# Optimization experiments

Hardware: AMD Instinct MI355X
Metric: run time of the kernel (lower is better)

## Reference

```python
import jax, jax.numpy as jnp
import numpy as np

LATENT = 768
HEADS = 12
HEAD_DIM = LATENT // HEADS
FFN = 4 * LATENT


def setup_inputs() -> dict:
    key = jax.random.key(0)
    ks = jax.random.split(key, 16)
    s = 1.0 / np.sqrt(LATENT)
    inp = {
        "x": jax.random.normal(ks[0], (2, 2048, LATENT), dtype=jnp.float32),
        "Wq": jax.random.normal(ks[1], (LATENT, LATENT), dtype=jnp.float32) * s,
        "bq": jnp.zeros((LATENT,), jnp.float32),
        "Wk": jax.random.normal(ks[2], (LATENT, LATENT), dtype=jnp.float32) * s,
        "bk": jnp.zeros((LATENT,), jnp.float32),
        "Wv": jax.random.normal(ks[3], (LATENT, LATENT), dtype=jnp.float32) * s,
        "bv": jnp.zeros((LATENT,), jnp.float32),
        "Wo": jax.random.normal(ks[4], (LATENT, LATENT), dtype=jnp.float32) * s,
        "bo": jnp.zeros((LATENT,), jnp.float32),
        "ln1_g": jnp.ones((LATENT,), jnp.float32),
        "ln1_b": jnp.zeros((LATENT,), jnp.float32),
        "ln2_g": jnp.ones((LATENT,), jnp.float32),
        "ln2_b": jnp.zeros((LATENT,), jnp.float32),
        "W1": jax.random.normal(ks[5], (FFN, LATENT), dtype=jnp.float32) * s,
        "b1": jnp.zeros((FFN,), jnp.float32),
        "W2": jax.random.normal(ks[6], (LATENT, FFN), dtype=jnp.float32) * (1.0 / np.sqrt(FFN)),
        "b2": jnp.zeros((LATENT,), jnp.float32),
    }
    return inp


def _layernorm(x, g, b, eps=1e-5):
    mu = jnp.mean(x, axis=-1, keepdims=True)
    var = jnp.var(x, axis=-1, keepdims=True)
    return (x - mu) * jax.lax.rsqrt(var + eps) * g + b


def reference(x, Wq, bq, Wk, bk, Wv, bv, Wo, bo, ln1_g, ln1_b, ln2_g, ln2_b, W1, b1, W2, b2):
    b, n, d = x.shape
    # torch Linear: y = x @ W.T + bias
    Q = (x @ Wq.T + bq).reshape(b, n, HEADS, HEAD_DIM).transpose(0, 2, 1, 3)
    K = (x @ Wk.T + bk).reshape(b, n, HEADS, HEAD_DIM).transpose(0, 2, 1, 3)
    V = (x @ Wv.T + bv).reshape(b, n, HEADS, HEAD_DIM).transpose(0, 2, 1, 3)
    scores = jnp.einsum("bhqd,bhkd->bhqk", Q, K) / np.sqrt(HEAD_DIM)  # [b,h,n,n]
    weights = jax.nn.softmax(scores, axis=-1)
    attn = jnp.einsum("bhqk,bhkd->bhqd", weights, V)
    attn = attn.transpose(0, 2, 1, 3).reshape(b, n, d)
    attn = attn @ Wo.T + bo
    x = _layernorm(x + attn, ln1_g, ln1_b)
    h = jax.nn.gelu(x @ W1.T + b1, approximate=False)
    ffn = h @ W2.T + b2
    x = _layernorm(x + ffn, ln2_g, ln2_b)
    return x
```

## Files before the change

kernel.cpp:

```cpp
#include <hip/hip_runtime.h>
#include <hip/hip_bf16.h>
#include <cstddef>
#include <cstdint>

typedef __bf16 bf16_t;
typedef bf16_t bf16x8 __attribute__((ext_vector_type(8)));
typedef bf16_t bf16x4 __attribute__((ext_vector_type(4)));
typedef float f32x4 __attribute__((ext_vector_type(4)));

#define LATENT 768
#define FFN_DIM 3072
#define NTOK 4096
#define SEQ 2048
#define HEADS 12
#define HD 64

__device__ __forceinline__ void gload_lds16(const bf16_t* g, bf16_t* l) {
    __builtin_amdgcn_global_load_lds((const __attribute__((address_space(1))) void*)g,
                                     (__attribute__((address_space(3))) void*)l, 16, 0, 0);
}

struct CvtDesc {
    const float* src[7];
    bf16_t* dst[7];
    int n4[7];
};

__global__ __launch_bounds__(256) void cvt_f32_bf16(CvtDesc d) {
    int seg = blockIdx.y;
    int i = blockIdx.x * 256 + threadIdx.x;
    if (i >= d.n4[seg]) return;
    float4 v = ((const float4*)d.src[seg])[i];
    bf16x4 o;
    o[0] = (bf16_t)v.x; o[1] = (bf16_t)v.y; o[2] = (bf16_t)v.z; o[3] = (bf16_t)v.w;
    *(bf16x4*)&d.dst[seg][(size_t)i * 4] = o;
}

template<int EPI, int NT>
__global__ __launch_bounds__(256) void gemm128(const bf16_t* __restrict__ A,
                                               const bf16_t* __restrict__ B,
                                               const float* __restrict__ bias,
                                               void* __restrict__ Cv,
                                               int M, int N, int K) {
    __shared__ __align__(16) bf16_t As[128 * 32];
    __shared__ __align__(16) bf16_t Bs[NT * 32];
    const int NJ = NT / 32;
    int t = threadIdx.x;
    int w = t >> 6;
    int lane = t & 63, l16 = lane & 15, quad = lane >> 4;
    int m0 = blockIdx.x * 128, n0 = blockIdx.y * NT;
    int mrow0 = (w & 1) * 64, ncol0 = (w >> 1) * (NT / 2);

    f32x4 acc[4][NJ] = {};

    int srow = lane >> 2;
    int sseg = (lane & 3) * 8;

    for (int k0 = 0; k0 < K; k0 += 32) {
        __syncthreads();
        const bf16_t* Ag = A + (size_t)(m0 + w * 32 + srow) * K + k0 + sseg;
        gload_lds16(Ag,          &As[(w * 32) * 32]);
        gload_lds16(Ag + 16 * K, &As[(w * 32 + 16) * 32]);
        if (NT == 128) {
            const bf16_t* Bg = B + (size_t)(n0 + w * 32 + srow) * K + k0 + sseg;
            gload_lds16(Bg,          &Bs[(w * 32) * 32]);
            gload_lds16(Bg + 16 * K, &Bs[(w * 32 + 16) * 32]);
        } else {
            const bf16_t* Bg = B + (size_t)(n0 + w * 16 + srow) * K + k0 + sseg;
            gload_lds16(Bg, &Bs[(w * 16) * 32]);
        }
        __syncthreads();

        bf16x8 a[4], b[NJ];
#pragma unroll
        for (int i = 0; i < 4; ++i)
            a[i] = *(const bf16x8*)&As[(mrow0 + i * 16 + l16) * 32 + quad * 8];
#pragma unroll
        for (int j = 0; j < NJ; ++j)
            b[j] = *(const bf16x8*)&Bs[(ncol0 + j * 16 + l16) * 32 + quad * 8];
#pragma unroll
        for (int i = 0; i < 4; ++i)
#pragma unroll
            for (int j = 0; j < NJ; ++j)
                acc[i][j] = __builtin_amdgcn_mfma_f32_16x16x32_bf16(a[i], b[j], acc[i][j], 0, 0, 0);
    }

    float* Cf = (float*)Cv;
    bf16_t* Cb = (bf16_t*)Cv;
#pragma unroll
    for (int j = 0; j < NJ; ++j) {
        int col = n0 + ncol0 + j * 16 + l16;
        float bvv = bias[col];
#pragma unroll
        for (int i = 0; i < 4; ++i) {
            int row0 = m0 + mrow0 + i * 16 + quad * 4;
#pragma unroll
            for (int r = 0; r < 4; ++r) {
                float v = acc[i][j][r] + bvv;
                if (EPI == 2) v = 0.5f * v * (1.0f + erff(v * 0.70710678118654752f));
                if (EPI == 0) Cf[(size_t)(row0 + r) * N + col] = v;
                else          Cb[(size_t)(row0 + r) * N + col] = (bf16_t)v;
            }
        }
    }
}

__global__ __launch_bounds__(256) void v_transpose(const bf16_t* __restrict__ QKV,
                                                   bf16_t* __restrict__ Vt) {
    __shared__ bf16_t Ts[64][68];
    int t = threadIdx.x;
    int bh = blockIdx.y;
    int b = bh / HEADS, h = bh % HEADS;
    int n0 = blockIdx.x * 64;
    size_t rowbase = (size_t)b * SEQ;
    int r = t >> 3, seg = (t & 7) * 8;
#pragma unroll
    for (int i = 0; i < 2; ++i) {
        int rr = r + i * 32;
        *(bf16x8*)&Ts[rr][seg] =
            *(const bf16x8*)&QKV[(rowbase + n0 + rr) * (3 * LATENT) + 2 * LATENT + h * HD + seg];
    }
    __syncthreads();
#pragma unroll
    for (int i = 0; i < 2; ++i) {
        int d = r + i * 32;
        bf16x8 o;
#pragma unroll
        for (int jj = 0; jj < 8; ++jj) o[jj] = Ts[seg + jj][d];
        *(bf16x8*)&Vt[((size_t)bh * HD + d) * SEQ + n0 + seg] = o;
    }
}

__global__ __launch_bounds__(256) void attn_flash(const bf16_t* __restrict__ QKV,
                                                  const bf16_t* __restrict__ Vt,
                                                  bf16_t* __restrict__ O) {
    __shared__ __align__(16) bf16_t Ks[2][64][32];
    __shared__ __align__(16) bf16_t Vts[2][64][32];
    __shared__ __align__(16) bf16_t Ps[4][32][72];

    int t = threadIdx.x;
    int w = t >> 6;
    int lane = t & 63, l16 = lane & 15, quad = lane >> 4;
    int bh = blockIdx.y;
    int b = bh / HEADS, h = bh % HEADS;
    size_t rowbase = (size_t)b * SEQ;
    int qw = blockIdx.x * 128 + w * 32;
    const int LD = 3 * LATENT;
    const float C2 = 0.125f * 1.44269504088896f;

    bf16x8 aq[2][2];
#pragma unroll
    for (int mi = 0; mi < 2; ++mi) {
        const bf16_t* qrow = QKV + (rowbase + qw + mi * 16 + l16) * LD + h * HD;
        aq[mi][0] = *(const bf16x8*)&qrow[quad * 8];
        aq[mi][1] = *(const bf16x8*)&qrow[32 + quad * 8];
    }

    f32x4 accd[2][4] = {};
    f32x4 vsum[2] = {};

    int c = w & 1, half = w >> 1;
    int srow = lane >> 2, sseg = (lane & 3) * 8;

    for (int kt = 0; kt < SEQ / 64; ++kt) {
        __syncthreads();
        {
            int krow = half * 32 + srow;
            const bf16_t* kg = QKV + (rowbase + kt * 64 + krow) * LD + LATENT + h * HD + c * 32 + sseg;
            gload_lds16(kg,           &Ks[c][half * 32][0]);
            gload_lds16(kg + 16 * LD, &Ks[c][half * 32 + 16][0]);
            const bf16_t* vg = Vt + ((size_t)bh * HD + half * 32 + srow) * SEQ + kt * 64 + c * 32 + sseg;
            gload_lds16(vg,            &Vts[c][half * 32][0]);
            gload_lds16(vg + 16 * SEQ, &Vts[c][half * 32 + 16][0]);
        }
        __syncthreads();

        bf16x8 bk[4][2];
#pragma unroll
        for (int si = 0; si < 4; ++si)
#pragma unroll
            for (int cc = 0; cc < 2; ++cc)
                bk[si][cc] = *(const bf16x8*)&Ks[cc][si * 16 + l16][quad * 8];

#pragma unroll
        for (int mi = 0; mi < 2; ++mi) {
#pragma unroll
            for (int si = 0; si < 4; ++si) {
                f32x4 z = {};
#pragma unroll
                for (int cc = 0; cc < 2; ++cc)
                    z = __builtin_amdgcn_mfma_f32_16x16x32_bf16(aq[mi][cc], bk[si][cc], z, 0, 0, 0);
#pragma unroll
                for (int r = 0; r < 4; ++r) {
                    float p = __builtin_amdgcn_exp2f(z[r] * C2);
                    vsum[mi][r] += p;
                    Ps[w][mi * 16 + quad * 4 + r][si * 16 + l16] = (bf16_t)p;
                }
            }
        }
        __threadfence_block();

        bf16x8 ap[2][2];
#pragma unroll
        for (int mi = 0; mi < 2; ++mi)
#pragma unroll
            for (int cc = 0; cc < 2; ++cc)
                ap[mi][cc] = *(const bf16x8*)&Ps[w][mi * 16 + l16][cc * 32 + quad * 8];

        bf16x8 bv[4][2];
#pragma unroll
        for (int dt = 0; dt < 4; ++dt)
#pragma unroll
            for (int cc = 0; cc < 2; ++cc)
                bv[dt][cc] = *(const bf16x8*)&Vts[cc][dt * 16 + l16][quad * 8];

#pragma unroll
        for (int mi = 0; mi < 2; ++mi)
#pragma unroll
            for (int dt = 0; dt < 4; ++dt)
#pragma unroll
                for (int cc = 0; cc < 2; ++cc)
                    accd[mi][dt] = __builtin_amdgcn_mfma_f32_16x16x32_bf16(ap[mi][cc], bv[dt][cc], accd[mi][dt], 0, 0, 0);
    }

#pragma unroll
    for (int mi = 0; mi < 2; ++mi) {
#pragma unroll
        for (int off = 1; off < 16; off <<= 1)
#pragma unroll
            for (int r = 0; r < 4; ++r) vsum[mi][r] += __shfl_xor(vsum[mi][r], off, 64);
    }
    f32x4 rinv[2];
#pragma unroll
    for (int mi = 0; mi < 2; ++mi)
#pragma unroll
        for (int r = 0; r < 4; ++r) rinv[mi][r] = 1.0f / vsum[mi][r];

#pragma unroll
    for (int mi = 0; mi < 2; ++mi)
#pragma unroll
        for (int dt = 0; dt < 4; ++dt)
#pragma unroll
            for (int r = 0; r < 4; ++r) {
                size_t row = rowbase + qw + mi * 16 + quad * 4 + r;
                O[row * LATENT + h * HD + dt * 16 + l16] = (bf16_t)(accd[mi][dt][r] * rinv[mi][r]);
            }
}

__global__ __launch_bounds__(256) void ln_residual(const float* __restrict__ base,
                                                   const float* __restrict__ add,
                                                   const float* __restrict__ g,
                                                   const float* __restrict__ bta,
                                                   float* __restrict__ outf,
                                                   bf16_t* __restrict__ outb) {
    int row = blockIdx.x;
    const float* xr = base + (size_t)row * LATENT;
    const float* ar = add + (size_t)row * LATENT;
    int t = threadIdx.x;
    float v[3];
    float s = 0.f;
#pragma unroll
    for (int i = 0; i < 3; ++i) {
        v[i] = xr[t + i * 256] + ar[t + i * 256];
        s += v[i];
    }
    __shared__ float red[4];
#pragma unroll
    for (int off = 1; off < 64; off <<= 1) s += __shfl_xor(s, off, 64);
    if ((t & 63) == 0) red[t >> 6] = s;
    __syncthreads();
    float mu = (red[0] + red[1] + red[2] + red[3]) * (1.f / LATENT);
    float q = 0.f;
#pragma unroll
    for (int i = 0; i < 3; ++i) {
        float d = v[i] - mu;
        q += d * d;
    }
#pragma unroll
    for (int off = 1; off < 64; off <<= 1) q += __shfl_xor(q, off, 64);
    __syncthreads();
    if ((t & 63) == 0) red[t >> 6] = q;
    __syncthreads();
    float var = (red[0] + red[1] + red[2] + red[3]) * (1.f / LATENT);
    float rs = rsqrtf(var + 1e-5f);
#pragma unroll
    for (int i = 0; i < 3; ++i) {
        int cix = t + i * 256;
        float o = (v[i] - mu) * rs * g[cix] + bta[cix];
        outf[(size_t)row * LATENT + cix] = o;
        if (outb) outb[(size_t)row * LATENT + cix] = (bf16_t)o;
    }
}

extern "C" void kernel_launch(void* const* d_in, const int* in_sizes, int n_in,
                              void* d_out, int out_size, void* d_ws, size_t ws_size,
                              hipStream_t stream) {
    const float* x   = (const float*)d_in[0];
    const float* Wq  = (const float*)d_in[1];
    const float* bq  = (const float*)d_in[2];
    const float* Wk  = (const float*)d_in[3];
    const float* bk  = (const float*)d_in[4];
    const float* Wv  = (const float*)d_in[5];
    const float* bv  = (const float*)d_in[6];
    const float* Wo  = (const float*)d_in[7];
    const float* bo  = (const float*)d_in[8];
    const float* g1  = (const float*)d_in[9];
    const float* be1 = (const float*)d_in[10];
    const float* g2  = (const float*)d_in[11];
    const float* be2 = (const float*)d_in[12];
    const float* W1  = (const float*)d_in[13];
    const float* b1  = (const float*)d_in[14];
    const float* W2  = (const float*)d_in[15];
    const float* b2  = (const float*)d_in[16];
    float* out = (float*)d_out;

    char* ws = (char*)d_ws;
    size_t off = 0;
    auto alloc = [&](size_t bytes) {
        char* p = ws + off;
        off = (off + bytes + 255) & ~(size_t)255;
        return p;
    };
    bf16_t* xbf   = (bf16_t*)alloc((size_t)NTOK * LATENT * 2);
    bf16_t* Wcat  = (bf16_t*)alloc((size_t)3 * LATENT * LATENT * 2);
    bf16_t* Wobf  = (bf16_t*)alloc((size_t)LATENT * LATENT * 2);
    bf16_t* W1bf  = (bf16_t*)alloc((size_t)FFN_DIM * LATENT * 2);
    bf16_t* W2bf  = (bf16_t*)alloc((size_t)LATENT * FFN_DIM * 2);
    float*  bcat  = (float*)alloc((size_t)3 * LATENT * 4);
    bf16_t* QKV   = (bf16_t*)alloc((size_t)NTOK * 3 * LATENT * 2);
    bf16_t* attnO = (bf16_t*)alloc((size_t)NTOK * LATENT * 2);
    float*  tmpf  = (float*)alloc((size_t)NTOK * LATENT * 4);
    float*  y1f   = (float*)alloc((size_t)NTOK * LATENT * 4);
    bf16_t* y1bf  = (bf16_t*)alloc((size_t)NTOK * LATENT * 2);
    bf16_t* hbf   = (bf16_t*)alloc((size_t)NTOK * FFN_DIM * 2);
    bf16_t* Vtg   = (bf16_t*)hbf;

    CvtDesc cd;
    cd.src[0] = x;   cd.dst[0] = xbf;                        cd.n4[0] = NTOK * LATENT / 4;
    cd.src[1] = Wq;  cd.dst[1] = Wcat;                       cd.n4[1] = LATENT * LATENT / 4;
    cd.src[2] = Wk;  cd.dst[2] = Wcat + LATENT * LATENT;     cd.n4[2] = LATENT * LATENT / 4;
    cd.src[3] = Wv;  cd.dst[3] = Wcat + 2 * LATENT * LATENT; cd.n4[3] = LATENT * LATENT / 4;
    cd.src[4] = Wo;  cd.dst[4] = Wobf;                       cd.n4[4] = LATENT * LATENT / 4;
    cd.src[5] = W1;  cd.dst[5] = W1bf;                       cd.n4[5] = FFN_DIM * LATENT / 4;
    cd.src[6] = W2;  cd.dst[6] = W2bf;                       cd.n4[6] = FFN_DIM * LATENT / 4;
    {
        int maxn4 = NTOK * LATENT / 4;
        dim3 grid((maxn4 + 255) / 256, 7);
        cvt_f32_bf16<<<grid, 256, 0, stream>>>(cd);
    }
    hipMemcpyAsync(bcat, bq, LATENT * 4, hipMemcpyDeviceToDevice, stream);
    hipMemcpyAsync(bcat + LATENT, bk, LATENT * 4, hipMemcpyDeviceToDevice, stream);
    hipMemcpyAsync(bcat + 2 * LATENT, bv, LATENT * 4, hipMemcpyDeviceToDevice, stream);

    gemm128<1, 128><<<dim3(NTOK / 128, 3 * LATENT / 128), 256, 0, stream>>>(
        xbf, Wcat, bcat, QKV, NTOK, 3 * LATENT, LATENT);

    v_transpose<<<dim3(SEQ / 64, 2 * HEADS), 256, 0, stream>>>(QKV, Vtg);

    attn_flash<<<dim3(SEQ / 128, 2 * HEADS), 256, 0, stream>>>(QKV, Vtg, attnO);

    gemm128<0, 64><<<dim3(NTOK / 128, LATENT / 64), 256, 0, stream>>>(
        attnO, Wobf, bo, tmpf, NTOK, LATENT, LATENT);

    ln_residual<<<NTOK, 256, 0, stream>>>(x, tmpf, g1, be1, y1f, y1bf);

    gemm128<2, 128><<<dim3(NTOK / 128, FFN_DIM / 128), 256, 0, stream>>>(
        y1bf, W1bf, b1, hbf, NTOK, FFN_DIM, LATENT);

    gemm128<0, 64><<<dim3(NTOK / 128, LATENT / 64), 256, 0, stream>>>(
        hbf, W2bf, b2, tmpf, NTOK, LATENT, FFN_DIM);

    ln_residual<<<NTOK, 256, 0, stream>>>(y1f, tmpf, g2, be2, out, nullptr);
}
```

Before: 338.2 us.

## Split attention KV range and output GEMMs along K into partial sums

```diff
diff --git a/kernel.cpp b/kernel.cpp
--- a/kernel.cpp
+++ b/kernel.cpp
@@ -41,7 +41,7 @@
                                                const bf16_t* __restrict__ B,
                                                const float* __restrict__ bias,
                                                void* __restrict__ Cv,
-                                               int M, int N, int K) {
+                                               int M, int N, int Klen, int Kstride) {
     __shared__ __align__(16) bf16_t As[128 * 32];
     __shared__ __align__(16) bf16_t Bs[NT * 32];
     const int NJ = NT / 32;
@@ -56,17 +56,17 @@
     int srow = lane >> 2;
     int sseg = (lane & 3) * 8;
 
-    for (int k0 = 0; k0 < K; k0 += 32) {
+    for (int k0 = 0; k0 < Klen; k0 += 32) {
         __syncthreads();
-        const bf16_t* Ag = A + (size_t)(m0 + w * 32 + srow) * K + k0 + sseg;
-        gload_lds16(Ag,          &As[(w * 32) * 32]);
-        gload_lds16(Ag + 16 * K, &As[(w * 32 + 16) * 32]);
+        const bf16_t* Ag = A + (size_t)(m0 + w * 32 + srow) * Kstride + k0 + sseg;
+        gload_lds16(Ag,                &As[(w * 32) * 32]);
+        gload_lds16(Ag + 16 * Kstride, &As[(w * 32 + 16) * 32]);
         if (NT == 128) {
-            const bf16_t* Bg = B + (size_t)(n0 + w * 32 + srow) * K + k0 + sseg;
-            gload_lds16(Bg,          &Bs[(w * 32) * 32]);
-            gload_lds16(Bg + 16 * K, &Bs[(w * 32 + 16) * 32]);
+            const bf16_t* Bg = B + (size_t)(n0 + w * 32 + srow) * Kstride + k0 + sseg;
+            gload_lds16(Bg,                &Bs[(w * 32) * 32]);
+            gload_lds16(Bg + 16 * Kstride, &Bs[(w * 32 + 16) * 32]);
         } else {
-            const bf16_t* Bg = B + (size_t)(n0 + w * 16 + srow) * K + k0 + sseg;
+            const bf16_t* Bg = B + (size_t)(n0 + w * 16 + srow) * Kstride + k0 + sseg;
             gload_lds16(Bg, &Bs[(w * 16) * 32]);
         }
         __syncthreads();
@@ -90,7 +90,7 @@
 #pragma unroll
     for (int j = 0; j < NJ; ++j) {
         int col = n0 + ncol0 + j * 16 + l16;
-        float bvv = bias[col];
+        float bvv = bias ? bias[col] : 0.0f;
 #pragma unroll
         for (int i = 0; i < 4; ++i) {
             int row0 = m0 + mrow0 + i * 16 + quad * 4;
@@ -133,7 +133,10 @@
 
 __global__ __launch_bounds__(256) void attn_flash(const bf16_t* __restrict__ QKV,
                                                   const bf16_t* __restrict__ Vt,
-                                                  bf16_t* __restrict__ O) {
+                                                  float* __restrict__ Op0,
+                                                  float* __restrict__ Op1,
+                                                  float* __restrict__ vs0,
+                                                  float* __restrict__ vs1) {
     __shared__ __align__(16) bf16_t Ks[2][64][32];
     __shared__ __align__(16) bf16_t Vts[2][64][32];
     __shared__ __align__(16) bf16_t Ps[4][32][72];
@@ -143,6 +146,9 @@
     int lane = t & 63, l16 = lane & 15, quad = lane >> 4;
     int bh = blockIdx.y;
     int b = bh / HEADS, h = bh % HEADS;
+    int z = blockIdx.z;
+    float* Op = z ? Op1 : Op0;
+    float* vs = z ? vs1 : vs0;
     size_t rowbase = (size_t)b * SEQ;
     int qw = blockIdx.x * 128 + w * 32;
     const int LD = 3 * LATENT;
@@ -162,7 +168,7 @@
     int c = w & 1, half = w >> 1;
     int srow = lane >> 2, sseg = (lane & 3) * 8;
 
-    for (int kt = 0; kt < SEQ / 64; ++kt) {
+    for (int kt = z * (SEQ / 128); kt < (z + 1) * (SEQ / 128); ++kt) {
         __syncthreads();
         {
             int krow = half * 32 + srow;
@@ -186,13 +192,13 @@
         for (int mi = 0; mi < 2; ++mi) {
 #pragma unroll
             for (int si = 0; si < 4; ++si) {
-                f32x4 z = {};
+                f32x4 z2 = {};
 #pragma unroll
                 for (int cc = 0; cc < 2; ++cc)
-                    z = __builtin_amdgcn_mfma_f32_16x16x32_bf16(aq[mi][cc], bk[si][cc], z, 0, 0, 0);
+                    z2 = __builtin_amdgcn_mfma_f32_16x16x32_bf16(aq[mi][cc], bk[si][cc], z2, 0, 0, 0);
 #pragma unroll
                 for (int r = 0; r < 4; ++r) {
-                    float p = __builtin_amdgcn_exp2f(z[r] * C2);
+                    float p = __builtin_amdgcn_exp2f(z2[r] * C2);
                     vsum[mi][r] += p;
                     Ps[w][mi * 16 + quad * 4 + r][si * 16 + l16] = (bf16_t)p;
                 }
@@ -229,12 +235,14 @@
         for (int off = 1; off < 16; off <<= 1)
 #pragma unroll
             for (int r = 0; r < 4; ++r) vsum[mi][r] += __shfl_xor(vsum[mi][r], off, 64);
-    }
-    f32x4 rinv[2];
-#pragma unroll
-    for (int mi = 0; mi < 2; ++mi)
-#pragma unroll
-        for (int r = 0; r < 4; ++r) rinv[mi][r] = 1.0f / vsum[mi][r];
+        if (l16 == 0) {
+#pragma unroll
+            for (int r = 0; r < 4; ++r) {
+                size_t tok = rowbase + qw + mi * 16 + quad * 4 + r;
+                vs[tok * HEADS + h] = vsum[mi][r];
+            }
+        }
+    }
 
 #pragma unroll
     for (int mi = 0; mi < 2; ++mi)
@@ -243,25 +251,46 @@
 #pragma unroll
             for (int r = 0; r < 4; ++r) {
                 size_t row = rowbase + qw + mi * 16 + quad * 4 + r;
-                O[row * LATENT + h * HD + dt * 16 + l16] = (bf16_t)(accd[mi][dt][r] * rinv[mi][r]);
+                Op[row * LATENT + h * HD + dt * 16 + l16] = accd[mi][dt][r];
             }
 }
 
-__global__ __launch_bounds__(256) void ln_residual(const float* __restrict__ base,
-                                                   const float* __restrict__ add,
-                                                   const float* __restrict__ g,
-                                                   const float* __restrict__ bta,
-                                                   float* __restrict__ outf,
-                                                   bf16_t* __restrict__ outb) {
+__global__ __launch_bounds__(256) void attn_combine(const float* __restrict__ Op0,
+                                                    const float* __restrict__ Op1,
+                                                    const float* __restrict__ vs0,
+                                                    const float* __restrict__ vs1,
+                                                    bf16_t* __restrict__ O) {
+    int row = blockIdx.x;
+    int t = threadIdx.x;
+    const float* a = Op0 + (size_t)row * LATENT;
+    const float* bb = Op1 + (size_t)row * LATENT;
+#pragma unroll
+    for (int i = 0; i < 3; ++i) {
+        int c = t + i * 256;
+        int h = c >> 6;
+        float denom = vs0[(size_t)row * HEADS + h] + vs1[(size_t)row * HEADS + h];
+        O[(size_t)row * LATENT + c] = (bf16_t)((a[c] + bb[c]) / denom);
+    }
+}
+
+__global__ __launch_bounds__(256) void ln_residual2(const float* __restrict__ base,
+                                                    const float* __restrict__ add1,
+                                                    const float* __restrict__ add2,
+                                                    const float* __restrict__ g,
+                                                    const float* __restrict__ bta,
+                                                    float* __restrict__ outf,
+                                                    bf16_t* __restrict__ outb) {
     int row = blockIdx.x;
     const float* xr = base + (size_t)row * LATENT;
-    const float* ar = add + (size_t)row * LATENT;
+    const float* a1 = add1 + (size_t)row * LATENT;
+    const float* a2 = add2 + (size_t)row * LATENT;
     int t = threadIdx.x;
     float v[3];
     float s = 0.f;
 #pragma unroll
     for (int i = 0; i < 3; ++i) {
-        v[i] = xr[t + i * 256] + ar[t + i * 256];
+        int c = t + i * 256;
+        v[i] = xr[c] + a1[c] + a2[c];
         s += v[i];
     }
     __shared__ float red[4];
@@ -333,7 +362,12 @@
     float*  y1f   = (float*)alloc((size_t)NTOK * LATENT * 4);
     bf16_t* y1bf  = (bf16_t*)alloc((size_t)NTOK * LATENT * 2);
     bf16_t* hbf   = (bf16_t*)alloc((size_t)NTOK * FFN_DIM * 2);
+    float*  vsa   = (float*)alloc((size_t)NTOK * HEADS * 4);
+    float*  vsb   = (float*)alloc((size_t)NTOK * HEADS * 4);
     bf16_t* Vtg   = (bf16_t*)hbf;
+    float*  Oa    = tmpf;
+    float*  Ob    = y1f;
+    float*  part2 = (float*)QKV;
 
     CvtDesc cd;
     cd.src[0] = x;   cd.dst[0] = xbf;                        cd.n4[0] = NTOK * LATENT / 4;
@@ -353,22 +387,28 @@
     hipMemcpyAsync(bcat + 2 * LATENT, bv, LATENT * 4, hipMemcpyDeviceToDevice, stream);
 
     gemm128<1, 128><<<dim3(NTOK / 128, 3 * LATENT / 128), 256, 0, stream>>>(
-        xbf, Wcat, bcat, QKV, NTOK, 3 * LATENT, LATENT);
+        xbf, Wcat, bcat, QKV, NTOK, 3 * LATENT, LATENT, LATENT);
 
     v_transpose<<<dim3(SEQ / 64, 2 * HEADS), 256, 0, stream>>>(QKV, Vtg);
 
-    attn_flash<<<dim3(SEQ / 128, 2 * HEADS), 256, 0, stream>>>(QKV, Vtg, attnO);
+    attn_flash<<<dim3(SEQ / 128, 2 * HEADS, 2), 256, 0, stream>>>(QKV, Vtg, Oa, Ob, vsa, vsb);
+
+    attn_combine<<<NTOK, 256, 0, stream>>>(Oa, Ob, vsa, vsb, attnO);
 
     gemm128<0, 64><<<dim3(NTOK / 128, LATENT / 64), 256, 0, stream>>>(
-        attnO, Wobf, bo, tmpf, NTOK, LATENT, LATENT);
-
-    ln_residual<<<NTOK, 256, 0, stream>>>(x, tmpf, g1, be1, y1f, y1bf);
+        attnO, Wobf, bo, tmpf, NTOK, LATENT, LATENT / 2, LATENT);
+    gemm128<0, 64><<<dim3(NTOK / 128, LATENT / 64), 256, 0, stream>>>(
+        attnO + LATENT / 2, Wobf + LATENT / 2, nullptr, part2, NTOK, LATENT, LATENT / 2, LATENT);
+
+    ln_residual2<<<NTOK, 256, 0, stream>>>(x, tmpf, part2, g1, be1, y1f, y1bf);
 
     gemm128<2, 128><<<dim3(NTOK / 128, FFN_DIM / 128), 256, 0, stream>>>(
-        y1bf, W1bf, b1, hbf, NTOK, FFN_DIM, LATENT);
+        y1bf, W1bf, b1, hbf, NTOK, FFN_DIM, LATENT, LATENT);
 
     gemm128<0, 64><<<dim3(NTOK / 128, LATENT / 64), 256, 0, stream>>>(
-        hbf, W2bf, b2, tmpf, NTOK, LATENT, FFN_DIM);
-
-    ln_residual<<<NTOK, 256, 0, stream>>>(y1f, tmpf, g2, be2, out, nullptr);
-}
+        hbf, W2bf, b2, tmpf, NTOK, LATENT, FFN_DIM / 2, FFN_DIM);
+    gemm128<0, 64><<<dim3(NTOK / 128, LATENT / 64), 256, 0, stream>>>(
+        hbf + FFN_DIM / 2, W2bf + FFN_DIM / 2, nullptr, part2, NTOK, LATENT, FFN_DIM / 2, FFN_DIM);
+
+    ln_residual2<<<NTOK, 256, 0, stream>>>(y1f, tmpf, part2, g2, be2, out, nullptr);
+}
```

Result: slower. 358.9 us (+6.1%).

## Split attention KV range across two blocks with single-wave blocks and combine pass

Applied to the files above, without the earlier changes.

```diff
diff --git a/kernel.cpp b/kernel.cpp
--- a/kernel.cpp
+++ b/kernel.cpp
@@ -131,20 +131,23 @@
     }
 }
 
-__global__ __launch_bounds__(256) void attn_flash(const bf16_t* __restrict__ QKV,
-                                                  const bf16_t* __restrict__ Vt,
-                                                  bf16_t* __restrict__ O) {
-    __shared__ __align__(16) bf16_t Ks[2][64][32];
-    __shared__ __align__(16) bf16_t Vts[2][64][32];
-    __shared__ __align__(16) bf16_t Ps[4][32][72];
-
-    int t = threadIdx.x;
-    int w = t >> 6;
-    int lane = t & 63, l16 = lane & 15, quad = lane >> 4;
-    int bh = blockIdx.y;
+__global__ __launch_bounds__(64, 4) void attn_flash(const bf16_t* __restrict__ QKV,
+                                                    const bf16_t* __restrict__ Vt,
+                                                    float* __restrict__ Op0,
+                                                    float* __restrict__ Op1,
+                                                    float* __restrict__ vs0,
+                                                    float* __restrict__ vs1) {
+    __shared__ __align__(16) bf16_t Ps[32][72];
+
+    int lane = threadIdx.x;
+    int l16 = lane & 15, quad = lane >> 4;
+    int bh = blockIdx.x;
     int b = bh / HEADS, h = bh % HEADS;
+    int qw = blockIdx.y * 32;
+    int z = blockIdx.z;
+    float* Op = z ? Op1 : Op0;
+    float* vs = z ? vs1 : vs0;
     size_t rowbase = (size_t)b * SEQ;
-    int qw = blockIdx.x * 128 + w * 32;
     const int LD = 3 * LATENT;
     const float C2 = 0.125f * 1.44269504088896f;
 
@@ -156,45 +159,46 @@
         aq[mi][1] = *(const bf16x8*)&qrow[32 + quad * 8];
     }
 
+    const bf16_t* kbase[4];
+    const bf16_t* vbase[4];
+#pragma unroll
+    for (int si = 0; si < 4; ++si)
+        kbase[si] = QKV + (rowbase + z * (SEQ / 2) + si * 16 + l16) * LD
+                        + LATENT + h * HD + quad * 8;
+#pragma unroll
+    for (int dt = 0; dt < 4; ++dt)
+        vbase[dt] = Vt + ((size_t)bh * HD + dt * 16 + l16) * SEQ
+                       + z * (SEQ / 2) + quad * 8;
+
     f32x4 accd[2][4] = {};
     f32x4 vsum[2] = {};
 
-    int c = w & 1, half = w >> 1;
-    int srow = lane >> 2, sseg = (lane & 3) * 8;
-
-    for (int kt = 0; kt < SEQ / 64; ++kt) {
-        __syncthreads();
-        {
-            int krow = half * 32 + srow;
-            const bf16_t* kg = QKV + (rowbase + kt * 64 + krow) * LD + LATENT + h * HD + c * 32 + sseg;
-            gload_lds16(kg,           &Ks[c][half * 32][0]);
-            gload_lds16(kg + 16 * LD, &Ks[c][half * 32 + 16][0]);
-            const bf16_t* vg = Vt + ((size_t)bh * HD + half * 32 + srow) * SEQ + kt * 64 + c * 32 + sseg;
-            gload_lds16(vg,            &Vts[c][half * 32][0]);
-            gload_lds16(vg + 16 * SEQ, &Vts[c][half * 32 + 16][0]);
-        }
-        __syncthreads();
-
-        bf16x8 bk[4][2];
-#pragma unroll
-        for (int si = 0; si < 4; ++si)
-#pragma unroll
-            for (int cc = 0; cc < 2; ++cc)
-                bk[si][cc] = *(const bf16x8*)&Ks[cc][si * 16 + l16][quad * 8];
+    for (int kt = 0; kt < SEQ / 128; ++kt) {
+        bf16x8 bk[4][2], bv[4][2];
+#pragma unroll
+        for (int si = 0; si < 4; ++si) {
+            bk[si][0] = *(const bf16x8*)(kbase[si]);
+            bk[si][1] = *(const bf16x8*)(kbase[si] + 32);
+        }
+#pragma unroll
+        for (int dt = 0; dt < 4; ++dt) {
+            bv[dt][0] = *(const bf16x8*)(vbase[dt]);
+            bv[dt][1] = *(const bf16x8*)(vbase[dt] + 32);
+        }
 
 #pragma unroll
         for (int mi = 0; mi < 2; ++mi) {
 #pragma unroll
             for (int si = 0; si < 4; ++si) {
-                f32x4 z = {};
+                f32x4 z2 = {};
 #pragma unroll
                 for (int cc = 0; cc < 2; ++cc)
-                    z = __builtin_amdgcn_mfma_f32_16x16x32_bf16(aq[mi][cc], bk[si][cc], z, 0, 0, 0);
+                    z2 = __builtin_amdgcn_mfma_f32_16x16x32_bf16(aq[mi][cc], bk[si][cc], z2, 0, 0, 0);
 #pragma unroll
                 for (int r = 0; r < 4; ++r) {
-                    float p = __builtin_amdgcn_exp2f(z[r] * C2);
+                    float p = __builtin_amdgcn_exp2f(z2[r] * C2);
                     vsum[mi][r] += p;
-                    Ps[w][mi * 16 + quad * 4 + r][si * 16 + l16] = (bf16_t)p;
+                    Ps[mi * 16 + quad * 4 + r][si * 16 + l16] = (bf16_t)p;
                 }
             }
         }
@@ -205,14 +209,7 @@
         for (int mi = 0; mi < 2; ++mi)
 #pragma unroll
             for (int cc = 0; cc < 2; ++cc)
-                ap[mi][cc] = *(const bf16x8*)&Ps[w][mi * 16 + l16][cc * 32 + quad * 8];
-
-        bf16x8 bv[4][2];
-#pragma unroll
-        for (int dt = 0; dt < 4; ++dt)
-#pragma unroll
-            for (int cc = 0; cc < 2; ++cc)
-                bv[dt][cc] = *(const bf16x8*)&Vts[cc][dt * 16 + l16][quad * 8];
+                ap[mi][cc] = *(const bf16x8*)&Ps[mi * 16 + l16][cc * 32 + quad * 8];
 
 #pragma unroll
         for (int mi = 0; mi < 2; ++mi)
@@ -221,6 +218,11 @@
 #pragma unroll
                 for (int cc = 0; cc < 2; ++cc)
                     accd[mi][dt] = __builtin_amdgcn_mfma_f32_16x16x32_bf16(ap[mi][cc], bv[dt][cc], accd[mi][dt], 0, 0, 0);
+
+#pragma unroll
+        for (int si = 0; si < 4; ++si) kbase[si] += 64 * LD;
+#pragma unroll
+        for (int dt = 0; dt < 4; ++dt) vbase[dt] += 64;
     }
 
 #pragma unroll
@@ -229,12 +231,14 @@
         for (int off = 1; off < 16; off <<= 1)
 #pragma unroll
             for (int r = 0; r < 4; ++r) vsum[mi][r] += __shfl_xor(vsum[mi][r], off, 64);
-    }
-    f32x4 rinv[2];
-#pragma unroll
-    for (int mi = 0; mi < 2; ++mi)
-#pragma unroll
-        for (int r = 0; r < 4; ++r) rinv[mi][r] = 1.0f / vsum[mi][r];
+        if (l16 == 0) {
+#pragma unroll
+            for (int r = 0; r < 4; ++r) {
+                size_t tok = rowbase + qw + mi * 16 + quad * 4 + r;
+                vs[tok * HEADS + h] = vsum[mi][r];
+            }
+        }
+    }
 
 #pragma unroll
     for (int mi = 0; mi < 2; ++mi)
@@ -243,8 +247,26 @@
 #pragma unroll
             for (int r = 0; r < 4; ++r) {
                 size_t row = rowbase + qw + mi * 16 + quad * 4 + r;
-                O[row * LATENT + h * HD + dt * 16 + l16] = (bf16_t)(accd[mi][dt][r] * rinv[mi][r]);
+                Op[row * LATENT + h * HD + dt * 16 + l16] = accd[mi][dt][r];
             }
+}
+
+__global__ __launch_bounds__(256) void attn_combine(const float* __restrict__ Op0,
+                                                    const float* __restrict__ Op1,
+                                                    const float* __restrict__ vs0,
+                                                    const float* __restrict__ vs1,
+                                                    bf16_t* __restrict__ O) {
+    int row = blockIdx.x;
+    int t = threadIdx.x;
+    const float* a = Op0 + (size_t)row * LATENT;
+    const float* bb = Op1 + (size_t)row * LATENT;
+#pragma unroll
+    for (int i = 0; i < 3; ++i) {
+        int c = t + i * 256;
+        int h = c >> 6;
+        float denom = vs0[(size_t)row * HEADS + h] + vs1[(size_t)row * HEADS + h];
+        O[(size_t)row * LATENT + c] = (bf16_t)((a[c] + bb[c]) / denom);
+    }
 }
 
 __global__ __launch_bounds__(256) void ln_residual(const float* __restrict__ base,
@@ -333,7 +355,11 @@
     float*  y1f   = (float*)alloc((size_t)NTOK * LATENT * 4);
     bf16_t* y1bf  = (bf16_t*)alloc((size_t)NTOK * LATENT * 2);
     bf16_t* hbf   = (bf16_t*)alloc((size_t)NTOK * FFN_DIM * 2);
+    float*  vsa   = (float*)alloc((size_t)NTOK * HEADS * 4);
+    float*  vsb   = (float*)alloc((size_t)NTOK * HEADS * 4);
     bf16_t* Vtg   = (bf16_t*)hbf;
+    float*  Oa    = tmpf;
+    float*  Ob    = y1f;
 
     CvtDesc cd;
     cd.src[0] = x;   cd.dst[0] = xbf;                        cd.n4[0] = NTOK * LATENT / 4;
@@ -357,7 +383,9 @@
 
     v_transpose<<<dim3(SEQ / 64, 2 * HEADS), 256, 0, stream>>>(QKV, Vtg);
 
-    attn_flash<<<dim3(SEQ / 128, 2 * HEADS), 256, 0, stream>>>(QKV, Vtg, attnO);
+    attn_flash<<<dim3(2 * HEADS, SEQ / 32, 2), 64, 0, stream>>>(QKV, Vtg, Oa, Ob, vsa, vsb);
+
+    attn_combine<<<NTOK, 256, 0, stream>>>(Oa, Ob, vsa, vsb, attnO);
 
     gemm128<0, 64><<<dim3(NTOK / 128, LATENT / 64), 256, 0, stream>>>(
         attnO, Wobf, bo, tmpf, NTOK, LATENT, LATENT);
```

Result: slower. 392.8 us (+16.2%).

## Restructure attention to single-wave blocks of 64 queries with head-major grid

Applied to the files above, without the earlier changes.

```diff
diff --git a/kernel.cpp b/kernel.cpp
--- a/kernel.cpp
+++ b/kernel.cpp
@@ -131,120 +131,107 @@
     }
 }
 
-__global__ __launch_bounds__(256) void attn_flash(const bf16_t* __restrict__ QKV,
-                                                  const bf16_t* __restrict__ Vt,
-                                                  bf16_t* __restrict__ O) {
+__global__ __launch_bounds__(64) void attn_flash(const bf16_t* __restrict__ QKV,
+                                                 const bf16_t* __restrict__ Vt,
+                                                 bf16_t* __restrict__ O) {
     __shared__ __align__(16) bf16_t Ks[2][64][32];
     __shared__ __align__(16) bf16_t Vts[2][64][32];
-    __shared__ __align__(16) bf16_t Ps[4][32][72];
-
-    int t = threadIdx.x;
-    int w = t >> 6;
-    int lane = t & 63, l16 = lane & 15, quad = lane >> 4;
-    int bh = blockIdx.y;
+    __shared__ __align__(16) bf16_t Ps[64][70];
+
+    int lane = threadIdx.x;
+    int l16 = lane & 15, quad = lane >> 4;
+    int bh = blockIdx.x;
     int b = bh / HEADS, h = bh % HEADS;
+    int qw = blockIdx.y * 64;
     size_t rowbase = (size_t)b * SEQ;
-    int qw = blockIdx.x * 128 + w * 32;
     const int LD = 3 * LATENT;
     const float C2 = 0.125f * 1.44269504088896f;
 
-    bf16x8 aq[2][2];
-#pragma unroll
-    for (int mi = 0; mi < 2; ++mi) {
+    bf16x8 aq[4][2];
+#pragma unroll
+    for (int mi = 0; mi < 4; ++mi) {
         const bf16_t* qrow = QKV + (rowbase + qw + mi * 16 + l16) * LD + h * HD;
         aq[mi][0] = *(const bf16x8*)&qrow[quad * 8];
         aq[mi][1] = *(const bf16x8*)&qrow[32 + quad * 8];
     }
 
-    f32x4 accd[2][4] = {};
-    f32x4 vsum[2] = {};
-
-    int c = w & 1, half = w >> 1;
-    int srow = lane >> 2, sseg = (lane & 3) * 8;
+    f32x4 accd[4][4] = {};
+    f32x4 vsum[4] = {};
+
+    int srow = lane >> 2;
+    int sseg = (lane & 3) * 8;
 
     for (int kt = 0; kt < SEQ / 64; ++kt) {
         __syncthreads();
-        {
-            int krow = half * 32 + srow;
-            const bf16_t* kg = QKV + (rowbase + kt * 64 + krow) * LD + LATENT + h * HD + c * 32 + sseg;
-            gload_lds16(kg,           &Ks[c][half * 32][0]);
-            gload_lds16(kg + 16 * LD, &Ks[c][half * 32 + 16][0]);
-            const bf16_t* vg = Vt + ((size_t)bh * HD + half * 32 + srow) * SEQ + kt * 64 + c * 32 + sseg;
-            gload_lds16(vg,            &Vts[c][half * 32][0]);
-            gload_lds16(vg + 16 * SEQ, &Vts[c][half * 32 + 16][0]);
+#pragma unroll
+        for (int g = 0; g < 4; ++g) {
+            const bf16_t* kg = QKV + (rowbase + kt * 64 + g * 16 + srow) * LD
+                                   + LATENT + h * HD + sseg;
+            gload_lds16(kg,      &Ks[0][g * 16][0]);
+            gload_lds16(kg + 32, &Ks[1][g * 16][0]);
+        }
+#pragma unroll
+        for (int g = 0; g < 4; ++g) {
+            const bf16_t* vg = Vt + ((size_t)bh * HD + g * 16 + srow) * SEQ
+                                  + kt * 64 + sseg;
+            gload_lds16(vg,      &Vts[0][g * 16][0]);
+            gload_lds16(vg + 32, &Vts[1][g * 16][0]);
         }
         __syncthreads();
 
-        bf16x8 bk[4][2];
-#pragma unroll
-        for (int si = 0; si < 4; ++si)
-#pragma unroll
-            for (int cc = 0; cc < 2; ++cc)
-                bk[si][cc] = *(const bf16x8*)&Ks[cc][si * 16 + l16][quad * 8];
-
-#pragma unroll
-        for (int mi = 0; mi < 2; ++mi) {
-#pragma unroll
-            for (int si = 0; si < 4; ++si) {
+#pragma unroll
+        for (int si = 0; si < 4; ++si) {
+            bf16x8 bk0 = *(const bf16x8*)&Ks[0][si * 16 + l16][quad * 8];
+            bf16x8 bk1 = *(const bf16x8*)&Ks[1][si * 16 + l16][quad * 8];
+#pragma unroll
+            for (int mi = 0; mi < 4; ++mi) {
                 f32x4 z = {};
-#pragma unroll
-                for (int cc = 0; cc < 2; ++cc)
-                    z = __builtin_amdgcn_mfma_f32_16x16x32_bf16(aq[mi][cc], bk[si][cc], z, 0, 0, 0);
+                z = __builtin_amdgcn_mfma_f32_16x16x32_bf16(aq[mi][0], bk0, z, 0, 0, 0);
+                z = __builtin_amdgcn_mfma_f32_16x16x32_bf16(aq[mi][1], bk1, z, 0, 0, 0);
 #pragma unroll
                 for (int r = 0; r < 4; ++r) {
                     float p = __builtin_amdgcn_exp2f(z[r] * C2);
                     vsum[mi][r] += p;
-                    Ps[w][mi * 16 + quad * 4 + r][si * 16 + l16] = (bf16_t)p;
+                    Ps[mi * 16 + quad * 4 + r][si * 16 + l16] = (bf16_t)p;
                 }
             }
         }
         __threadfence_block();
 
-        bf16x8 ap[2][2];
-#pragma unroll
-        for (int mi = 0; mi < 2; ++mi)
-#pragma unroll
-            for (int cc = 0; cc < 2; ++cc)
-                ap[mi][cc] = *(const bf16x8*)&Ps[w][mi * 16 + l16][cc * 32 + quad * 8];
-
-        bf16x8 bv[4][2];
-#pragma unroll
-        for (int dt = 0; dt < 4; ++dt)
-#pragma unroll
-            for (int cc = 0; cc < 2; ++cc)
-                bv[dt][cc] = *(const bf16x8*)&Vts[cc][dt * 16 + l16][quad * 8];
-
-#pragma unroll
-        for (int mi = 0; mi < 2; ++mi)
-#pragma unroll
-            for (int dt = 0; dt < 4; ++dt)
-#pragma unroll
-                for (int cc = 0; cc < 2; ++cc)
-                    accd[mi][dt] = __builtin_amdgcn_mfma_f32_16x16x32_bf16(ap[mi][cc], bv[dt][cc], accd[mi][dt], 0, 0, 0);
-    }
-
-#pragma unroll
-    for (int mi = 0; mi < 2; ++mi) {
+#pragma unroll
+        for (int dt = 0; dt < 4; ++dt) {
+            bf16x8 bv0 = *(const bf16x8*)&Vts[0][dt * 16 + l16][quad * 8];
+            bf16x8 bv1 = *(const bf16x8*)&Vts[1][dt * 16 + l16][quad * 8];
+#pragma unroll
+            for (int mi = 0; mi < 4; ++mi) {
+                bf16x8 ap0 = *(const bf16x8*)&Ps[mi * 16 + l16][quad * 8];
+                bf16x8 ap1 = *(const bf16x8*)&Ps[mi * 16 + l16][32 + quad * 8];
+                accd[mi][dt] = __builtin_amdgcn_mfma_f32_16x16x32_bf16(ap0, bv0, accd[mi][dt], 0, 0, 0);
+                accd[mi][dt] = __builtin_amdgcn_mfma_f32_16x16x32_bf16(ap1, bv1, accd[mi][dt], 0, 0, 0);
+            }
+        }
+    }
+
+#pragma unroll
+    for (int mi = 0; mi < 4; ++mi) {
 #pragma unroll
         for (int off = 1; off < 16; off <<= 1)
 #pragma unroll
             for (int r = 0; r < 4; ++r) vsum[mi][r] += __shfl_xor(vsum[mi][r], off, 64);
     }
-    f32x4 rinv[2];
-#pragma unroll
-    for (int mi = 0; mi < 2; ++mi)
-#pragma unroll
-        for (int r = 0; r < 4; ++r) rinv[mi][r] = 1.0f / vsum[mi][r];
-
-#pragma unroll
-    for (int mi = 0; mi < 2; ++mi)
+#pragma unroll
+    for (int mi = 0; mi < 4; ++mi) {
+        f32x4 rinv;
+#pragma unroll
+        for (int r = 0; r < 4; ++r) rinv[r] = 1.0f / vsum[mi][r];
 #pragma unroll
         for (int dt = 0; dt < 4; ++dt)
 #pragma unroll
             for (int r = 0; r < 4; ++r) {
                 size_t row = rowbase + qw + mi * 16 + quad * 4 + r;
-                O[row * LATENT + h * HD + dt * 16 + l16] = (bf16_t)(accd[mi][dt][r] * rinv[mi][r]);
+                O[row * LATENT + h * HD + dt * 16 + l16] = (bf16_t)(accd[mi][dt][r] * rinv[r]);
             }
+    }
 }
 
 __global__ __launch_bounds__(256) void ln_residual(const float* __restrict__ base,
@@ -357,7 +344,7 @@
 
     v_transpose<<<dim3(SEQ / 64, 2 * HEADS), 256, 0, stream>>>(QKV, Vtg);
 
-    attn_flash<<<dim3(SEQ / 128, 2 * HEADS), 256, 0, stream>>>(QKV, Vtg, attnO);
+    attn_flash<<<dim3(2 * HEADS, SEQ / 64), 64, 0, stream>>>(QKV, Vtg, attnO);
 
     gemm128<0, 64><<<dim3(NTOK / 128, LATENT / 64), 256, 0, stream>>>(
         attnO, Wobf, bo, tmpf, NTOK, LATENT, LATENT);
```

Result: slower. 352.7 us (+4.3%).
